# Performance work log

Measured on AMD Instinct MI355X. Metric: run time of the kernel, lower is better.

The kernel has to match this reference:

```python
import jax, jax.numpy as jnp
import numpy as np
from jax import lax

TH = 1.0  # fire threshold (init kwarg th)


def setup_inputs() -> dict:
    key = jax.random.key(0)
    k0, k1, k2 = jax.random.split(key, 3)
    B, T, C = 32, 3000, 512
    hs_pad = jax.random.normal(k0, (B, T, C), dtype=jnp.float32)
    hs_mask = jnp.ones((B, 1, T), dtype=jnp.int32)  # espnet-style [B,1,T] mask, 1=valid
    # Conv1d(C, C, k=5) weight layout [out, in, k], fan-in scaled
    conv_w = jax.random.normal(k1, (C, C, 5), dtype=jnp.float32) * (1.0 / np.sqrt(C * 5))
    conv_b = jnp.zeros((C,), dtype=jnp.float32)
    # Linear(C, 1): stored transposed as [C, 1]
    lin_w = jax.random.normal(k2, (C, 1), dtype=jnp.float32) * (1.0 / np.sqrt(C))
    lin_b = jnp.zeros((1,), dtype=jnp.float32)
    return dict(hs_pad=hs_pad, hs_mask=hs_mask, conv_w=conv_w, conv_b=conv_b,
                lin_w=lin_w, lin_b=lin_b)


def _cif_single(alpha, h, th):
    """Integrate-and-fire for one sequence. alpha:[T], h:[T,C] -> [T,C] (zero padded)."""
    T, C = h.shape

    def step(carry, inp):
        acc, hacc = carry
        a, hu = inp
        acc2 = acc + a
        fired = acc2 >= th
        a1 = th - acc  # = th - (acc2 - a)
        emit = jnp.where(fired, hacc + a1 * hu, jnp.zeros_like(hu))
        new_acc = jnp.where(fired, a - a1, acc2)
        new_h = jnp.where(fired, (a - a1) * hu, hacc + a * hu)
        return (new_acc, new_h), (fired, emit)

    (acc_f, h_f), (fired, emits) = lax.scan(
        step, (jnp.float32(0.0), jnp.zeros((C,), h.dtype)), (alpha, h))
    nfire = jnp.cumsum(fired.astype(jnp.int32))
    idx = jnp.where(fired, nfire - 1, T)  # non-fired steps dump into scratch row T
    out = jnp.zeros((T + 1, C), h.dtype).at[idx].add(emits)
    # tail emission: remaining mass >= th/2
    tail = acc_f >= th * 0.5
    tail_idx = jnp.where(tail, nfire[-1], T)
    out = out.at[tail_idx].add(jnp.where(tail, h_f, jnp.zeros_like(h_f)))
    return out[:T]  # fires <= T always (alpha < 1 = th)


def _forward(hs_pad, hs_mask, conv_w, conv_b, lin_w, lin_b):
    B, T, C = hs_pad.shape
    # Conv1d(C,C,5,pad=2) on [B,C,T]  (note: self.norm is never used in the torch forward)
    x = lax.conv_general_dilated(hs_pad.transpose(0, 2, 1), conv_w, (1,), [(2, 2)],
                                 dimension_numbers=('NCH', 'OIH', 'NCH'))
    x = jax.nn.relu(x + conv_b[None, :, None])  # [B,C,T]
    alpha = jax.nn.sigmoid(jnp.einsum('bct,co->bto', x, lin_w) + lin_b)  # [B,T,1]
    # ys_pad=None -> T_y = 0; loss computed BEFORE masking (as in torch)
    loss_pen = jnp.abs(alpha.sum(axis=1) - 0.0).sum()
    a = alpha[..., 0] * (hs_mask[:, 0, :] != 0).astype(alpha.dtype)  # masked_fill(mask==0, 0)
    cs = jax.vmap(lambda av, hv: _cif_single(av, hv, TH))(a, hs_pad)  # [B,T,C]
    cs_mask = jnp.any(cs != 0.0, axis=-1)[:, None, :]  # [B,1,T]
    return cs, cs_mask, loss_pen


def reference(hs_pad, hs_mask, conv_w, conv_b, lin_w, lin_b):
    return _forward(hs_pad, hs_mask, conv_w, conv_b, lin_w, lin_b)
```

## Files before the change

kernel.cpp:

```cpp
#include <hip/hip_runtime.h>
#include <math.h>

#define B_ 32
#define T_ 3000
#define C_ 512
#define THf 1.0f
#define KW 2560

typedef _Float16 f16;
typedef _Float16 half8 __attribute__((ext_vector_type(8)));
typedef float floatx4 __attribute__((ext_vector_type(4)));

#define GLOBAL_AS __attribute__((address_space(1)))
#define LDS_AS __attribute__((address_space(3)))

#define CS_SIZE  ((size_t)B_ * T_ * C_)
#define MASK_OFF CS_SIZE
#define LOSS_OFF (CS_SIZE + (size_t)B_ * T_)

#define HS16_ELEMS   ((size_t)B_ * 16 * 3000 * 64)
#define HS16_ZEL     HS16_ELEMS
#define HS16_BYTES   (2 * (HS16_ELEMS + 64))
#define A_WHI_OFF    HS16_BYTES
#define A_WLO_OFF    (A_WHI_OFF + 2621440)
#define A_PL_OFF     (A_WLO_OFF + 2621440)
#define A_ALPHA_OFF  (A_PL_OFF + 3072000)
#define A_SEGI_OFF   (A_ALPHA_OFF + 384000)
#define A_SEGW_OFF   (A_SEGI_OFF + 768000)
#define A_TOT_OFF    (A_SEGW_OFF + 768000)
#define A_WS_NEED    (A_TOT_OFF + 128)

#define B_WHI_OFF   0
#define B_WLO_OFF   2621440
#define B_PL_OFF    5242880
#define B_ALPHA_OFF 8314880
#define B_SEGI_OFF  8698880
#define B_SEGW_OFF  9466880
#define B_TOT_OFF   10234880

__global__ __launch_bounds__(256) void w_prep_kernel(
    const float* __restrict__ W, f16* __restrict__ whi, f16* __restrict__ wlo)
{
    int idx = blockIdx.x * 256 + threadIdx.x;
    if (idx >= 512 * KW) return;
    int ie = idx & 7;
    int o  = (idx >> 3) & 511;
    int i8 = (idx >> 12) & 63;
    int k  = idx >> 18;
    int i  = i8 * 8 + ie;
    float w = W[o * KW + i * 5 + k];
    f16 h = (f16)w;
    whi[idx] = h;
    wlo[idx] = (f16)((w - (float)h) * 2048.0f);
}

__global__ __launch_bounds__(256) void hs_split_kernel(
    const float* __restrict__ hs, f16* __restrict__ hs16)
{
    int idx = blockIdx.x * 256 + threadIdx.x;
    if (idx < 8) {
        half8 z = {(f16)0.f, (f16)0.f, (f16)0.f, (f16)0.f,
                   (f16)0.f, (f16)0.f, (f16)0.f, (f16)0.f};
        *(half8*)(hs16 + HS16_ZEL + idx * 8) = z;
    }
    if (idx >= B_ * 16 * 3000 * 4) return;
    int ch  = idx & 3;
    int row = idx >> 2;
    int t   = row % 3000;
    int bic = row / 3000;
    int b   = bic >> 4;
    int ic  = bic & 15;
    const float* src = hs + ((size_t)b * 3000 + t) * 512 + ic * 32 + ch * 8;
    float4 v0 = *(const float4*)src;
    float4 v1 = *(const float4*)(src + 4);
    float vv[8] = {v0.x, v0.y, v0.z, v0.w, v1.x, v1.y, v1.z, v1.w};
    half8 hh, ll;
#pragma unroll
    for (int q = 0; q < 8; ++q) {
        f16 x = (f16)vv[q];
        hh[q] = x;
        ll[q] = (f16)((vv[q] - (float)x) * 2048.f);
    }
    int m7 = (t + 2) & 7;
    size_t rb = (size_t)row * 64;
    *(half8*)(hs16 + rb + (size_t)((ch ^ m7) * 8))       = hh;
    *(half8*)(hs16 + rb + (size_t)(((ch + 4) ^ m7) * 8)) = ll;
}

__global__ __launch_bounds__(256, 2) void conv_alpha_mfma_a(
    const f16* __restrict__ hs16, const f16* __restrict__ whi_g,
    const f16* __restrict__ wlo_g, const float* __restrict__ conv_b,
    const float* __restrict__ lin_w, float* __restrict__ pl)
{
    __shared__ f16 sm[33792];

    int tid = threadIdx.x;
    int bid = blockIdx.x;
    int nb  = bid & 3;
    int mtg = bid >> 2;
    int b   = mtg / 24;
    int mt  = mtg - b * 24;
    int t0  = mt * 128;

    int wid = tid >> 6, l = tid & 63;
    int wm = wid >> 1, wn = wid & 1;
    int l15 = l & 15, l4 = l >> 4;
    int o0 = nb * 128;

    floatx4 acc1[4][4], acc2[4][4];
#pragma unroll
    for (int mf = 0; mf < 4; ++mf)
#pragma unroll
        for (int nf = 0; nf < 4; ++nf) {
            acc1[mf][nf] = (floatx4)0.f;
            acc2[mf][nf] = (floatx4)0.f;
        }

    auto issue_a = [&](int icn) {
        const f16* hbase = hs16 + ((size_t)(b * 16 + icn)) * 3000 * 64;
        f16* abase = sm + (icn & 1) * 8704;
#pragma unroll
        for (int jj = 0; jj < 4; ++jj) {
            int j = wid + jj * 4;
            int r = j * 8 + (l >> 3);
            int t = t0 - 2 + r;
            const f16* gsrc = ((unsigned)t < 3000u)
                ? hbase + (size_t)t * 64 + (l & 7) * 8
                : hs16 + HS16_ZEL + (l & 7) * 8;
            __builtin_amdgcn_global_load_lds((const GLOBAL_AS void*)gsrc,
                                             (LDS_AS void*)(abase + j * 512), 16, 0, 0);
        }
        {
            int j = (wid == 0) ? 16 : (wid + 12);
            int r = j * 8 + (l >> 3);
            int t = t0 - 2 + r;
            const f16* gsrc = ((unsigned)t < 3000u)
                ? hbase + (size_t)t * 64 + (l & 7) * 8
                : hs16 + HS16_ZEL + (l & 7) * 8;
            __builtin_amdgcn_global_load_lds((const GLOBAL_AS void*)gsrc,
                                             (LDS_AS void*)(abase + j * 512), 16, 0, 0);
        }
    };
    auto issue_w = [&](int s2) {
        int buf = s2 & 1;
        int ic2 = s2 / 5, k2 = s2 - ic2 * 5;
#pragma unroll
        for (int rr = 0; rr < 4; ++rr) {
            int r = wid * 4 + rr;
            int arr = r >> 3, kc = (r >> 1) & 3, oh = r & 1;
            const f16* gsrc = (arr ? wlo_g : whi_g) +
                ((size_t)((k2 * 64 + ic2 * 4 + kc) * 512 + o0 + oh * 64 + l)) * 8;
            f16* ldst = sm + 17408 + (buf * 2 + arr) * 4096 + (kc * 128 + oh * 64) * 8;
            __builtin_amdgcn_global_load_lds((const GLOBAL_AS void*)gsrc,
                                             (LDS_AS void*)ldst, 16, 0, 0);
        }
    };

    issue_a(0);
    issue_w(0);
    __syncthreads();

    for (int s = 0; s < 80; ++s) {
        int ic = s / 5, k = s - ic * 5;
        int abuf = ic & 1, wbuf = s & 1;
        bool aStep = (k == 0) && (ic + 1 < 16);

        if (s + 1 < 80) issue_w(s + 1);
        if (aStep) issue_a(ic + 1);

        const f16* Ab = sm + abuf * 8704;
        const f16* Wh = sm + 17408 + (wbuf * 2 + 0) * 4096;
        const f16* Wl = sm + 17408 + (wbuf * 2 + 1) * 4096;
        int m7 = (l15 + k) & 7;
        int sh = (l4 ^ m7) * 8;
        int sl = ((l4 + 4) ^ m7) * 8;

        half8 ah[4], al[4], bh[4], bl[4];
#pragma unroll
        for (int f = 0; f < 4; ++f) {
            int r = wm * 64 + f * 16 + l15 + k;
            ah[f] = *(const half8*)(Ab + r * 64 + sh);
            al[f] = *(const half8*)(Ab + r * 64 + sl);
            int wrow = l4 * 128 + wn * 64 + f * 16 + l15;
            bh[f] = *(const half8*)(Wh + wrow * 8);
            bl[f] = *(const half8*)(Wl + wrow * 8);
        }
        __builtin_amdgcn_s_setprio(1);
#pragma unroll
        for (int mf = 0; mf < 4; ++mf)
#pragma unroll
            for (int nf = 0; nf < 4; ++nf) {
                acc1[mf][nf] = __builtin_amdgcn_mfma_f32_16x16x32_f16(
                    ah[mf], bh[nf], acc1[mf][nf], 0, 0, 0);
                acc2[mf][nf] = __builtin_amdgcn_mfma_f32_16x16x32_f16(
                    al[mf], bh[nf], acc2[mf][nf], 0, 0, 0);
                acc2[mf][nf] = __builtin_amdgcn_mfma_f32_16x16x32_f16(
                    ah[mf], bl[nf], acc2[mf][nf], 0, 0, 0);
            }
        __builtin_amdgcn_s_setprio(0);

        if (aStep) {
            asm volatile("s_waitcnt vmcnt(5)" ::: "memory");
            __builtin_amdgcn_s_barrier();
            __builtin_amdgcn_sched_barrier(0);
        } else {
            __syncthreads();
        }
    }

    float cb[4], lw[4];
#pragma unroll
    for (int nf = 0; nf < 4; ++nf) {
        int o = o0 + wn * 64 + nf * 16 + l15;
        cb[nf] = conv_b[o];
        lw[nf] = lin_w[o];
    }
    float* plb = pl + (size_t)(nb * 2 + wn) * (B_ * T_) + b * T_;
#pragma unroll
    for (int mf = 0; mf < 4; ++mf) {
#pragma unroll
        for (int reg = 0; reg < 4; ++reg) {
            float v = 0.f;
#pragma unroll
            for (int nf = 0; nf < 4; ++nf) {
                float c = acc1[mf][nf][reg] + acc2[mf][nf][reg] * (1.0f / 2048.0f);
                v += fmaxf(c + cb[nf], 0.f) * lw[nf];
            }
            v += __shfl_xor(v, 1);
            v += __shfl_xor(v, 2);
            v += __shfl_xor(v, 4);
            v += __shfl_xor(v, 8);
            int trow = t0 + wm * 64 + mf * 16 + l4 * 4 + reg;
            if (l15 == reg && trow < T_) plb[trow] = v;
        }
    }
}

#define A_ROWS 132
#define ALO_OFF_E  8448
#define WB_OFF_E   16896
#define WB_ARR_E   4096

__global__ __launch_bounds__(256, 2) void conv_alpha_mfma_b(
    const float* __restrict__ hs, const f16* __restrict__ whi_g,
    const f16* __restrict__ wlo_g, const float* __restrict__ conv_b,
    const float* __restrict__ lin_w, float* __restrict__ pl)
{
    __shared__ f16 sm[33280];
    f16* Ahi = sm;
    f16* Alo = sm + ALO_OFF_E;
    f16* Wb  = sm + WB_OFF_E;

    int tid = threadIdx.x;
    int bid = blockIdx.x;
    int nb  = bid & 3;
    int mtg = bid >> 2;
    int b   = mtg / 24;
    int mt  = mtg - b * 24;
    int t0  = mt * 128;

    int wid = tid >> 6, l = tid & 63;
    int wm = wid >> 1, wn = wid & 1;
    int l15 = l & 15, l4 = l >> 4;

    const float* hb = hs + (size_t)b * T_ * C_;
    int o0 = nb * 128;

    floatx4 acc1[4][4], acc2[4][4];
#pragma unroll
    for (int mf = 0; mf < 4; ++mf)
#pragma unroll
        for (int nf = 0; nf < 4; ++nf) {
            acc1[mf][nf] = (floatx4)0.f;
            acc2[mf][nf] = (floatx4)0.f;
        }

    auto issue_w = [&](int s2) {
        int buf = s2 & 1;
        int ic2 = s2 / 10, kk2 = s2 % 10;
        int k2 = kk2 >> 1, sub2 = kk2 & 1;
        int i8b = ic2 * 8 + sub2 * 4;
#pragma unroll
        for (int rr = 0; rr < 4; ++rr) {
            int r = wid * 4 + rr;
            int arr = r >> 3, kc = (r >> 1) & 3, oh = r & 1;
            const f16* gsrc = (arr ? wlo_g : whi_g) +
                ((size_t)((k2 * 64 + i8b + kc) * 512 + o0 + oh * 64 + l)) * 8;
            f16* ldst = Wb + (buf * 2 + arr) * WB_ARR_E + (kc * 128 + oh * 64) * 8;
            __builtin_amdgcn_global_load_lds((const GLOBAL_AS void*)gsrc,
                                             (LDS_AS void*)ldst, 16, 0, 0);
        }
    };

    issue_w(0);

    for (int s = 0; s < 80; ++s) {
        int ic = s / 10, kk = s % 10;
        int k = kk >> 1, sub = kk & 1;
        int buf = s & 1;

        if (kk == 0) {
            int i0 = ic * 64;
            for (int j = tid; j < A_ROWS * 8; j += 256) {
                int r = j >> 3, c = j & 7;
                int t = t0 - 2 + r;
                float4 v0 = make_float4(0.f, 0.f, 0.f, 0.f);
                float4 v1 = v0;
                if ((unsigned)t < (unsigned)T_) {
                    const float4* p = (const float4*)(hb + (size_t)t * C_ + i0 + c * 8);
                    v0 = p[0]; v1 = p[1];
                }
                float vv[8] = {v0.x, v0.y, v0.z, v0.w, v1.x, v1.y, v1.z, v1.w};
                half8 hh, ll;
#pragma unroll
                for (int q = 0; q < 8; ++q) {
                    f16 x = (f16)vv[q];
                    hh[q] = x;
                    ll[q] = (f16)((vv[q] - (float)x) * 2048.f);
                }
                int off = r * 64 + (c ^ (r & 7)) * 8;
                *(half8*)(Ahi + off) = hh;
                *(half8*)(Alo + off) = ll;
            }
            __syncthreads();
        }

        if (s + 1 < 80) issue_w(s + 1);

        half8 ah[4], al[4], bh[4], bl[4];
#pragma unroll
        for (int f = 0; f < 4; ++f) {
            int ar = wm * 64 + f * 16 + l15 + k;
            int aoff = ar * 64 + ((((sub << 2) | l4) ^ (ar & 7)) << 3);
            ah[f] = *(const half8*)(Ahi + aoff);
            al[f] = *(const half8*)(Alo + aoff);
            int wrow = l4 * 128 + wn * 64 + f * 16 + l15;
            bh[f] = *(const half8*)(Wb + (buf * 2 + 0) * WB_ARR_E + wrow * 8);
            bl[f] = *(const half8*)(Wb + (buf * 2 + 1) * WB_ARR_E + wrow * 8);
        }
        __builtin_amdgcn_s_setprio(1);
#pragma unroll
        for (int mf = 0; mf < 4; ++mf)
#pragma unroll
            for (int nf = 0; nf < 4; ++nf) {
                acc1[mf][nf] = __builtin_amdgcn_mfma_f32_16x16x32_f16(
                    ah[mf], bh[nf], acc1[mf][nf], 0, 0, 0);
                acc2[mf][nf] = __builtin_amdgcn_mfma_f32_16x16x32_f16(
                    al[mf], bh[nf], acc2[mf][nf], 0, 0, 0);
                acc2[mf][nf] = __builtin_amdgcn_mfma_f32_16x16x32_f16(
                    ah[mf], bl[nf], acc2[mf][nf], 0, 0, 0);
            }
        __builtin_amdgcn_s_setprio(0);
        __syncthreads();
    }

    float cb[4], lw[4];
#pragma unroll
    for (int nf = 0; nf < 4; ++nf) {
        int o = o0 + wn * 64 + nf * 16 + l15;
        cb[nf] = conv_b[o];
        lw[nf] = lin_w[o];
    }
    float* plb = pl + (size_t)(nb * 2 + wn) * (B_ * T_) + b * T_;
#pragma unroll
    for (int mf = 0; mf < 4; ++mf) {
#pragma unroll
        for (int reg = 0; reg < 4; ++reg) {
            float v = 0.f;
#pragma unroll
            for (int nf = 0; nf < 4; ++nf) {
                float c = acc1[mf][nf][reg] + acc2[mf][nf][reg] * (1.0f / 2048.0f);
                v += fmaxf(c + cb[nf], 0.f) * lw[nf];
            }
            v += __shfl_xor(v, 1);
            v += __shfl_xor(v, 2);
            v += __shfl_xor(v, 4);
            v += __shfl_xor(v, 8);
            int trow = t0 + wm * 64 + mf * 16 + l4 * 4 + reg;
            if (l15 == reg && trow < T_) plb[trow] = v;
        }
    }
}

__global__ __launch_bounds__(256) void alpha_combine_kernel(
    const float* __restrict__ pl, const float* __restrict__ lin_b,
    float* __restrict__ alpha)
{
    int idx = blockIdx.x * 256 + threadIdx.x;
    if (idx >= B_ * T_) return;
    float s = lin_b[0];
#pragma unroll
    for (int p = 0; p < 8; ++p) s += pl[(size_t)p * (B_ * T_) + idx];
    alpha[idx] = 1.f / (1.f + expf(-s));
}

__global__ __launch_bounds__(64) void scan_kernel(
    float* __restrict__ alpha, const int* __restrict__ mask,
    int2* __restrict__ seg_i, float2* __restrict__ seg_w,
    int* __restrict__ total_rows, float* __restrict__ out_loss)
{
    int lane = threadIdx.x;
    float lsum = 0.f;
    if (lane < B_) {
        const float4* ap = (const float4*)(alpha + lane * T_);
        const int4*   mp = (const int4*)(mask + lane * T_);
        float* astore = alpha + lane * T_;
        int2*   si = seg_i + lane * T_;
        float2* sw = seg_w + lane * T_;

        float acc = 0.f, leftover = 0.f;
        int nf = 0, prev_t = -1;

        float4 c0 = ap[0], c1 = ap[1];
        int4   m0 = mp[0], m1 = mp[1];
        for (int tc = 0; tc < T_ / 8; ++tc) {
            float4 n0, n1; int4 nm0, nm1;
            if (tc + 1 < T_ / 8) {
                n0 = ap[(tc + 1) * 2]; n1 = ap[(tc + 1) * 2 + 1];
                nm0 = mp[(tc + 1) * 2]; nm1 = mp[(tc + 1) * 2 + 1];
            }
            float av[8] = {c0.x, c0.y, c0.z, c0.w, c1.x, c1.y, c1.z, c1.w};
            int   mv[8] = {m0.x, m0.y, m0.z, m0.w, m1.x, m1.y, m1.z, m1.w};
#pragma unroll
            for (int u = 0; u < 8; ++u) {
                int t = tc * 8 + u;
                float araw = av[u];
                lsum += araw;
                float a = (mv[u] != 0) ? araw : 0.f;
                astore[t] = a;
                float acc2 = acc + a;
                float a1 = THf - acc;
                if (acc2 >= THf) {
                    si[nf] = make_int2(prev_t, t);
                    sw[nf] = make_float2(leftover, a1);
                    float rem = a - a1;
                    leftover = rem;
                    acc = rem;
                    prev_t = t;
                    ++nf;
                } else {
                    acc = acc2;
                }
            }
            c0 = n0; c1 = n1; m0 = nm0; m1 = nm1;
        }
        int tot = nf;
        if (acc >= 0.5f * THf) {
            si[nf] = make_int2(prev_t, T_);
            sw[nf] = make_float2(leftover, 0.f);
            ++tot;
        }
        total_rows[lane] = tot;
        lsum = fabsf(lsum);
    }
#pragma unroll
    for (int off = 16; off >= 1; off >>= 1) lsum += __shfl_down(lsum, off);
    if (lane == 0) out_loss[0] = lsum;
}

__global__ __launch_bounds__(128) void emit_kernel(
    const float* __restrict__ hs, const float* __restrict__ alpha,
    const int2* __restrict__ seg_i, const float2* __restrict__ seg_w,
    const int* __restrict__ total_rows, float* __restrict__ out)
{
    int blk = blockIdx.x;
    int b = blk / T_;
    int r = blk % T_;
    int tid = threadIdx.x;

    float4* cs4 = (float4*)(out + ((size_t)b * T_ + r) * C_);
    float* maskp = out + MASK_OFF + (size_t)b * T_ + r;
    int tot = total_rows[b];

    if (r >= tot) {
        float4 z; z.x = 0.f; z.y = 0.f; z.z = 0.f; z.w = 0.f;
        cs4[tid] = z;
        if (tid == 0) *maskp = 0.f;
        return;
    }
    int2   si = seg_i[b * T_ + r];
    float2 sw = seg_w[b * T_ + r];
    const float4* hb = (const float4*)(hs + (size_t)b * T_ * C_);
    const float*  ab = alpha + b * T_;

    float4 acc; acc.x = 0.f; acc.y = 0.f; acc.z = 0.f; acc.w = 0.f;
    int ts = si.x, te = si.y;
    if (ts >= 0) {
        float4 h = hb[(size_t)ts * (C_ / 4) + tid];
        acc.x = sw.x * h.x; acc.y = sw.x * h.y; acc.z = sw.x * h.z; acc.w = sw.x * h.w;
    }
    for (int t = ts + 1; t < te; ++t) {
        float a = ab[t];
        float4 h = hb[(size_t)t * (C_ / 4) + tid];
        acc.x = fmaf(a, h.x, acc.x); acc.y = fmaf(a, h.y, acc.y);
        acc.z = fmaf(a, h.z, acc.z); acc.w = fmaf(a, h.w, acc.w);
    }
    if (te < T_) {
        float4 h = hb[(size_t)te * (C_ / 4) + tid];
        acc.x = fmaf(sw.y, h.x, acc.x); acc.y = fmaf(sw.y, h.y, acc.y);
        acc.z = fmaf(sw.y, h.z, acc.z); acc.w = fmaf(sw.y, h.w, acc.w);
    }
    cs4[tid] = acc;
    if (tid == 0) *maskp = 1.f;
}

extern "C" void kernel_launch(void* const* d_in, const int* in_sizes, int n_in,
                              void* d_out, int out_size, void* d_ws, size_t ws_size,
                              hipStream_t stream)
{
    const float* hs     = (const float*)d_in[0];
    const int*   hmask  = (const int*)d_in[1];
    const float* conv_w = (const float*)d_in[2];
    const float* conv_b = (const float*)d_in[3];
    const float* lin_w  = (const float*)d_in[4];
    const float* lin_b  = (const float*)d_in[5];
    float* out = (float*)d_out;
    char*  ws  = (char*)d_ws;

    if (ws_size >= (size_t)A_WS_NEED) {
        f16*    hs16  = (f16*)ws;
        f16*    whi   = (f16*)(ws + A_WHI_OFF);
        f16*    wlo   = (f16*)(ws + A_WLO_OFF);
        float*  pl    = (float*)(ws + A_PL_OFF);
        float*  alpha = (float*)(ws + A_ALPHA_OFF);
        int2*   seg_i = (int2*)(ws + A_SEGI_OFF);
        float2* seg_w = (float2*)(ws + A_SEGW_OFF);
        int*    tot   = (int*)(ws + A_TOT_OFF);

        w_prep_kernel<<<(512 * KW + 255) / 256, 256, 0, stream>>>(conv_w, whi, wlo);
        hs_split_kernel<<<(B_ * 16 * 3000 * 4 + 255) / 256, 256, 0, stream>>>(hs, hs16);
        conv_alpha_mfma_a<<<B_ * 24 * 4, 256, 0, stream>>>(hs16, whi, wlo, conv_b,
                                                           lin_w, pl);
        alpha_combine_kernel<<<(B_ * T_ + 255) / 256, 256, 0, stream>>>(pl, lin_b, alpha);
        scan_kernel<<<1, 64, 0, stream>>>(alpha, hmask, seg_i, seg_w, tot, out + LOSS_OFF);
        emit_kernel<<<B_ * T_, 128, 0, stream>>>(hs, alpha, seg_i, seg_w, tot, out);
    } else {
        f16*    whi   = (f16*)(ws + B_WHI_OFF);
        f16*    wlo   = (f16*)(ws + B_WLO_OFF);
        float*  pl    = (float*)(ws + B_PL_OFF);
        float*  alpha = (float*)(ws + B_ALPHA_OFF);
        int2*   seg_i = (int2*)(ws + B_SEGI_OFF);
        float2* seg_w = (float2*)(ws + B_SEGW_OFF);
        int*    tot   = (int*)(ws + B_TOT_OFF);

        w_prep_kernel<<<(512 * KW + 255) / 256, 256, 0, stream>>>(conv_w, whi, wlo);
        conv_alpha_mfma_b<<<B_ * 24 * 4, 256, 0, stream>>>(hs, whi, wlo, conv_b,
                                                           lin_w, pl);
        alpha_combine_kernel<<<(B_ * T_ + 255) / 256, 256, 0, stream>>>(pl, lin_b, alpha);
        scan_kernel<<<1, 64, 0, stream>>>(alpha, hmask, seg_i, seg_w, tot, out + LOSS_OFF);
        emit_kernel<<<B_ * T_, 128, 0, stream>>>(hs, alpha, seg_i, seg_w, tot, out);
    }
}
```

Baseline: 994.4 us.

## Switch conv MFMA to 32x32x16 tiles with single accumulator and occupancy 3

```diff
diff --git a/kernel.cpp b/kernel.cpp
--- a/kernel.cpp
+++ b/kernel.cpp
@@ -10,6 +10,7 @@
 typedef _Float16 f16;
 typedef _Float16 half8 __attribute__((ext_vector_type(8)));
 typedef float floatx4 __attribute__((ext_vector_type(4)));
+typedef float floatx16 __attribute__((ext_vector_type(16)));
 
 #define GLOBAL_AS __attribute__((address_space(1)))
 #define LDS_AS __attribute__((address_space(3)))
@@ -17,6 +18,8 @@
 #define CS_SIZE  ((size_t)B_ * T_ * C_)
 #define MASK_OFF CS_SIZE
 #define LOSS_OFF (CS_SIZE + (size_t)B_ * T_)
+
+#define LOSC 64.0f
 
 #define HS16_ELEMS   ((size_t)B_ * 16 * 3000 * 64)
 #define HS16_ZEL     HS16_ELEMS
@@ -51,7 +54,7 @@
     float w = W[o * KW + i * 5 + k];
     f16 h = (f16)w;
     whi[idx] = h;
-    wlo[idx] = (f16)((w - (float)h) * 2048.0f);
+    wlo[idx] = (f16)((w - (float)h) * LOSC);
 }
 
 __global__ __launch_bounds__(256) void hs_split_kernel(
@@ -79,7 +82,7 @@
     for (int q = 0; q < 8; ++q) {
         f16 x = (f16)vv[q];
         hh[q] = x;
-        ll[q] = (f16)((vv[q] - (float)x) * 2048.f);
+        ll[q] = (f16)((vv[q] - (float)x) * LOSC);
     }
     int m7 = (t + 2) & 7;
     size_t rb = (size_t)row * 64;
@@ -87,12 +90,12 @@
     *(half8*)(hs16 + rb + (size_t)(((ch + 4) ^ m7) * 8)) = ll;
 }
 
-__global__ __launch_bounds__(256, 2) void conv_alpha_mfma_a(
+__global__ __launch_bounds__(256, 3) void conv_alpha_mfma_a(
     const f16* __restrict__ hs16, const f16* __restrict__ whi_g,
     const f16* __restrict__ wlo_g, const float* __restrict__ conv_b,
     const float* __restrict__ lin_w, float* __restrict__ pl)
 {
-    __shared__ f16 sm[33792];
+    __shared__ f16 sm[25600];
 
     int tid = threadIdx.x;
     int bid = blockIdx.x;
@@ -104,17 +107,14 @@
 
     int wid = tid >> 6, l = tid & 63;
     int wm = wid >> 1, wn = wid & 1;
-    int l15 = l & 15, l4 = l >> 4;
+    int l31 = l & 31, l5 = l >> 5;
     int o0 = nb * 128;
 
-    floatx4 acc1[4][4], acc2[4][4];
-#pragma unroll
-    for (int mf = 0; mf < 4; ++mf)
-#pragma unroll
-        for (int nf = 0; nf < 4; ++nf) {
-            acc1[mf][nf] = (floatx4)0.f;
-            acc2[mf][nf] = (floatx4)0.f;
-        }
+    floatx16 acc[2][2];
+#pragma unroll
+    for (int mf = 0; mf < 2; ++mf)
+#pragma unroll
+        for (int nf = 0; nf < 2; ++nf) acc[mf][nf] = (floatx16)0.f;
 
     auto issue_a = [&](int icn) {
         const f16* hbase = hs16 + ((size_t)(b * 16 + icn)) * 3000 * 64;
@@ -142,15 +142,16 @@
         }
     };
     auto issue_w = [&](int s2) {
-        int buf = s2 & 1;
-        int ic2 = s2 / 5, k2 = s2 - ic2 * 5;
-#pragma unroll
-        for (int rr = 0; rr < 4; ++rr) {
-            int r = wid * 4 + rr;
-            int arr = r >> 3, kc = (r >> 1) & 3, oh = r & 1;
-            const f16* gsrc = (arr ? wlo_g : whi_g) +
-                ((size_t)((k2 * 64 + ic2 * 4 + kc) * 512 + o0 + oh * 64 + l)) * 8;
-            f16* ldst = sm + 17408 + (buf * 2 + arr) * 4096 + (kc * 128 + oh * 64) * 8;
+        int wbuf2 = s2 & 1;
+        int ic2 = s2 / 10, kk2 = s2 % 10;
+        int k2 = kk2 >> 1, h2 = kk2 & 1;
+        int g0 = ic2 * 4 + h2 * 2;
+        int g = wid >> 1, oh = wid & 1;
+#pragma unroll
+        for (int v = 0; v < 2; ++v) {
+            const f16* gsrc = (v ? wlo_g : whi_g) +
+                ((size_t)((k2 * 64 + g0 + g) * 512 + o0 + oh * 64 + l)) * 8;
+            f16* ldst = sm + 17408 + wbuf2 * 4096 + ((v * 2 + g) * 128 + oh * 64) * 8;
             __builtin_amdgcn_global_load_lds((const GLOBAL_AS void*)gsrc,
                                              (LDS_AS void*)ldst, 16, 0, 0);
         }
@@ -160,78 +161,72 @@
     issue_w(0);
     __syncthreads();
 
-    for (int s = 0; s < 80; ++s) {
-        int ic = s / 5, k = s - ic * 5;
+    const f16 inv64 = (f16)(1.0f / 64.0f);
+
+    for (int s = 0; s < 160; ++s) {
+        int ic = s / 10, kk = s % 10;
+        int k = kk >> 1, h = kk & 1;
         int abuf = ic & 1, wbuf = s & 1;
-        bool aStep = (k == 0) && (ic + 1 < 16);
-
-        if (s + 1 < 80) issue_w(s + 1);
-        if (aStep) issue_a(ic + 1);
+
+        if (s + 1 < 160) issue_w(s + 1);
+        if (kk == 0 && ic + 1 < 16) issue_a(ic + 1);
 
         const f16* Ab = sm + abuf * 8704;
-        const f16* Wh = sm + 17408 + (wbuf * 2 + 0) * 4096;
-        const f16* Wl = sm + 17408 + (wbuf * 2 + 1) * 4096;
-        int m7 = (l15 + k) & 7;
-        int sh = (l4 ^ m7) * 8;
-        int sl = ((l4 + 4) ^ m7) * 8;
-
-        half8 ah[4], al[4], bh[4], bl[4];
-#pragma unroll
-        for (int f = 0; f < 4; ++f) {
-            int r = wm * 64 + f * 16 + l15 + k;
-            ah[f] = *(const half8*)(Ab + r * 64 + sh);
-            al[f] = *(const half8*)(Ab + r * 64 + sl);
-            int wrow = l4 * 128 + wn * 64 + f * 16 + l15;
-            bh[f] = *(const half8*)(Wh + wrow * 8);
-            bl[f] = *(const half8*)(Wl + wrow * 8);
-        }
+        const f16* Wb = sm + 17408 + wbuf * 4096;
+        int chh = h * 2 + l5;
+
+        half8 ah[2], al[2], bh[2], bl[2];
+#pragma unroll
+        for (int f = 0; f < 2; ++f) {
+            int r = wm * 64 + f * 32 + l31 + k;
+            int sw = r & 7;
+            ah[f] = *(const half8*)(Ab + r * 64 + ((chh ^ sw) << 3));
+            al[f] = *(const half8*)(Ab + r * 64 + (((chh + 4) ^ sw) << 3));
+            int oin = wn * 64 + f * 32 + l31;
+            bh[f] = *(const half8*)(Wb + (l5 * 128 + oin) * 8);
+            bl[f] = *(const half8*)(Wb + ((2 + l5) * 128 + oin) * 8);
+        }
+        half8 ahd[2], bhd[2];
+#pragma unroll
+        for (int f = 0; f < 2; ++f) { ahd[f] = ah[f] * inv64; bhd[f] = bh[f] * inv64; }
+
         __builtin_amdgcn_s_setprio(1);
 #pragma unroll
-        for (int mf = 0; mf < 4; ++mf)
-#pragma unroll
-            for (int nf = 0; nf < 4; ++nf) {
-                acc1[mf][nf] = __builtin_amdgcn_mfma_f32_16x16x32_f16(
-                    ah[mf], bh[nf], acc1[mf][nf], 0, 0, 0);
-                acc2[mf][nf] = __builtin_amdgcn_mfma_f32_16x16x32_f16(
-                    al[mf], bh[nf], acc2[mf][nf], 0, 0, 0);
-                acc2[mf][nf] = __builtin_amdgcn_mfma_f32_16x16x32_f16(
-                    ah[mf], bl[nf], acc2[mf][nf], 0, 0, 0);
+        for (int mf = 0; mf < 2; ++mf)
+#pragma unroll
+            for (int nf = 0; nf < 2; ++nf) {
+                acc[mf][nf] = __builtin_amdgcn_mfma_f32_32x32x16_f16(
+                    ah[mf], bh[nf], acc[mf][nf], 0, 0, 0);
+                acc[mf][nf] = __builtin_amdgcn_mfma_f32_32x32x16_f16(
+                    al[mf], bhd[nf], acc[mf][nf], 0, 0, 0);
+                acc[mf][nf] = __builtin_amdgcn_mfma_f32_32x32x16_f16(
+                    ahd[mf], bl[nf], acc[mf][nf], 0, 0, 0);
             }
         __builtin_amdgcn_s_setprio(0);
-
-        if (aStep) {
-            asm volatile("s_waitcnt vmcnt(5)" ::: "memory");
-            __builtin_amdgcn_s_barrier();
-            __builtin_amdgcn_sched_barrier(0);
-        } else {
-            __syncthreads();
-        }
-    }
-
-    float cb[4], lw[4];
-#pragma unroll
-    for (int nf = 0; nf < 4; ++nf) {
-        int o = o0 + wn * 64 + nf * 16 + l15;
+        __syncthreads();
+    }
+
+    float cb[2], lw[2];
+#pragma unroll
+    for (int nf = 0; nf < 2; ++nf) {
+        int o = o0 + wn * 64 + nf * 32 + l31;
         cb[nf] = conv_b[o];
         lw[nf] = lin_w[o];
     }
     float* plb = pl + (size_t)(nb * 2 + wn) * (B_ * T_) + b * T_;
 #pragma unroll
-    for (int mf = 0; mf < 4; ++mf) {
-#pragma unroll
-        for (int reg = 0; reg < 4; ++reg) {
-            float v = 0.f;
-#pragma unroll
-            for (int nf = 0; nf < 4; ++nf) {
-                float c = acc1[mf][nf][reg] + acc2[mf][nf][reg] * (1.0f / 2048.0f);
-                v += fmaxf(c + cb[nf], 0.f) * lw[nf];
-            }
+    for (int mf = 0; mf < 2; ++mf) {
+#pragma unroll
+        for (int r = 0; r < 16; ++r) {
+            float v = fmaxf(acc[mf][0][r] + cb[0], 0.f) * lw[0]
+                    + fmaxf(acc[mf][1][r] + cb[1], 0.f) * lw[1];
             v += __shfl_xor(v, 1);
             v += __shfl_xor(v, 2);
             v += __shfl_xor(v, 4);
             v += __shfl_xor(v, 8);
-            int trow = t0 + wm * 64 + mf * 16 + l4 * 4 + reg;
-            if (l15 == reg && trow < T_) plb[trow] = v;
+            v += __shfl_xor(v, 16);
+            int trow = t0 + wm * 64 + mf * 32 + l5 * 4 + (r & 3) + 8 * (r >> 2);
+            if (l31 == 0 && trow < T_) plb[trow] = v;
         }
     }
 }
@@ -316,7 +311,7 @@
                 for (int q = 0; q < 8; ++q) {
                     f16 x = (f16)vv[q];
                     hh[q] = x;
-                    ll[q] = (f16)((vv[q] - (float)x) * 2048.f);
+                    ll[q] = (f16)((vv[q] - (float)x) * LOSC);
                 }
                 int off = r * 64 + (c ^ (r & 7)) * 8;
                 *(half8*)(Ahi + off) = hh;
@@ -369,7 +364,7 @@
             float v = 0.f;
 #pragma unroll
             for (int nf = 0; nf < 4; ++nf) {
-                float c = acc1[mf][nf][reg] + acc2[mf][nf][reg] * (1.0f / 2048.0f);
+                float c = acc1[mf][nf][reg] + acc2[mf][nf][reg] * (1.0f / LOSC);
                 v += fmaxf(c + cb[nf], 0.f) * lw[nf];
             }
             v += __shfl_xor(v, 1);
```

Measured after the change: 1.153 ms. 1.16x slower.

## Merge split-fp16 accumulators and single-buffer A tile to raise conv kernel occupancy

Applied to the files above, without the earlier changes.

```diff
diff --git a/kernel.cpp b/kernel.cpp
--- a/kernel.cpp
+++ b/kernel.cpp
@@ -17,6 +17,8 @@
 #define CS_SIZE  ((size_t)B_ * T_ * C_)
 #define MASK_OFF CS_SIZE
 #define LOSS_OFF (CS_SIZE + (size_t)B_ * T_)
+
+#define LOSC 64.0f
 
 #define HS16_ELEMS   ((size_t)B_ * 16 * 3000 * 64)
 #define HS16_ZEL     HS16_ELEMS
@@ -51,7 +53,7 @@
     float w = W[o * KW + i * 5 + k];
     f16 h = (f16)w;
     whi[idx] = h;
-    wlo[idx] = (f16)((w - (float)h) * 2048.0f);
+    wlo[idx] = (f16)((w - (float)h) * LOSC);
 }
 
 __global__ __launch_bounds__(256) void hs_split_kernel(
@@ -79,7 +81,7 @@
     for (int q = 0; q < 8; ++q) {
         f16 x = (f16)vv[q];
         hh[q] = x;
-        ll[q] = (f16)((vv[q] - (float)x) * 2048.f);
+        ll[q] = (f16)((vv[q] - (float)x) * LOSC);
     }
     int m7 = (t + 2) & 7;
     size_t rb = (size_t)row * 64;
@@ -87,12 +89,12 @@
     *(half8*)(hs16 + rb + (size_t)(((ch + 4) ^ m7) * 8)) = ll;
 }
 
-__global__ __launch_bounds__(256, 2) void conv_alpha_mfma_a(
+__global__ __launch_bounds__(256, 3) void conv_alpha_mfma_a(
     const f16* __restrict__ hs16, const f16* __restrict__ whi_g,
     const f16* __restrict__ wlo_g, const float* __restrict__ conv_b,
     const float* __restrict__ lin_w, float* __restrict__ pl)
 {
-    __shared__ f16 sm[33792];
+    __shared__ f16 sm[25088];
 
     int tid = threadIdx.x;
     int bid = blockIdx.x;
@@ -107,18 +109,15 @@
     int l15 = l & 15, l4 = l >> 4;
     int o0 = nb * 128;
 
-    floatx4 acc1[4][4], acc2[4][4];
+    floatx4 acc[4][4];
 #pragma unroll
     for (int mf = 0; mf < 4; ++mf)
 #pragma unroll
-        for (int nf = 0; nf < 4; ++nf) {
-            acc1[mf][nf] = (floatx4)0.f;
-            acc2[mf][nf] = (floatx4)0.f;
-        }
+        for (int nf = 0; nf < 4; ++nf) acc[mf][nf] = (floatx4)0.f;
 
     auto issue_a = [&](int icn) {
         const f16* hbase = hs16 + ((size_t)(b * 16 + icn)) * 3000 * 64;
-        f16* abase = sm + (icn & 1) * 8704;
+        f16* abase = sm;
 #pragma unroll
         for (int jj = 0; jj < 4; ++jj) {
             int j = wid + jj * 4;
@@ -150,7 +149,7 @@
             int arr = r >> 3, kc = (r >> 1) & 3, oh = r & 1;
             const f16* gsrc = (arr ? wlo_g : whi_g) +
                 ((size_t)((k2 * 64 + ic2 * 4 + kc) * 512 + o0 + oh * 64 + l)) * 8;
-            f16* ldst = sm + 17408 + (buf * 2 + arr) * 4096 + (kc * 128 + oh * 64) * 8;
+            f16* ldst = sm + 8704 + (buf * 2 + arr) * 4096 + (kc * 128 + oh * 64) * 8;
             __builtin_amdgcn_global_load_lds((const GLOBAL_AS void*)gsrc,
                                              (LDS_AS void*)ldst, 16, 0, 0);
         }
@@ -160,17 +159,18 @@
     issue_w(0);
     __syncthreads();
 
+    const f16 inv64 = (f16)0.015625f;
+
     for (int s = 0; s < 80; ++s) {
         int ic = s / 5, k = s - ic * 5;
-        int abuf = ic & 1, wbuf = s & 1;
-        bool aStep = (k == 0) && (ic + 1 < 16);
-
-        if (s + 1 < 80) issue_w(s + 1);
-        if (aStep) issue_a(ic + 1);
-
-        const f16* Ab = sm + abuf * 8704;
-        const f16* Wh = sm + 17408 + (wbuf * 2 + 0) * 4096;
-        const f16* Wl = sm + 17408 + (wbuf * 2 + 1) * 4096;
+        int wbuf = s & 1;
+        bool aStep = (k == 4);
+
+        if (!aStep && s + 1 < 80) issue_w(s + 1);
+
+        const f16* Ab = sm;
+        const f16* Wh = sm + 8704 + (wbuf * 2 + 0) * 4096;
+        const f16* Wl = sm + 8704 + (wbuf * 2 + 1) * 4096;
         int m7 = (l15 + k) & 7;
         int sh = (l4 ^ m7) * 8;
         int sl = ((l4 + 4) ^ m7) * 8;
@@ -185,24 +185,31 @@
             bh[f] = *(const half8*)(Wh + wrow * 8);
             bl[f] = *(const half8*)(Wl + wrow * 8);
         }
+        half8 bhd[4];
+#pragma unroll
+        for (int nf = 0; nf < 4; ++nf) bhd[nf] = bh[nf] * inv64;
+
         __builtin_amdgcn_s_setprio(1);
 #pragma unroll
-        for (int mf = 0; mf < 4; ++mf)
+        for (int mf = 0; mf < 4; ++mf) {
+            half8 ahd = ah[mf] * inv64;
 #pragma unroll
             for (int nf = 0; nf < 4; ++nf) {
-                acc1[mf][nf] = __builtin_amdgcn_mfma_f32_16x16x32_f16(
-                    ah[mf], bh[nf], acc1[mf][nf], 0, 0, 0);
-                acc2[mf][nf] = __builtin_amdgcn_mfma_f32_16x16x32_f16(
-                    al[mf], bh[nf], acc2[mf][nf], 0, 0, 0);
-                acc2[mf][nf] = __builtin_amdgcn_mfma_f32_16x16x32_f16(
-                    ah[mf], bl[nf], acc2[mf][nf], 0, 0, 0);
-            }
+                acc[mf][nf] = __builtin_amdgcn_mfma_f32_16x16x32_f16(
+                    ah[mf], bh[nf], acc[mf][nf], 0, 0, 0);
+                acc[mf][nf] = __builtin_amdgcn_mfma_f32_16x16x32_f16(
+                    al[mf], bhd[nf], acc[mf][nf], 0, 0, 0);
+                acc[mf][nf] = __builtin_amdgcn_mfma_f32_16x16x32_f16(
+                    ahd, bl[nf], acc[mf][nf], 0, 0, 0);
+            }
+        }
         __builtin_amdgcn_s_setprio(0);
 
         if (aStep) {
-            asm volatile("s_waitcnt vmcnt(5)" ::: "memory");
-            __builtin_amdgcn_s_barrier();
-            __builtin_amdgcn_sched_barrier(0);
+            __syncthreads();
+            if (ic + 1 < 16) issue_a(ic + 1);
+            if (s + 1 < 80) issue_w(s + 1);
+            __syncthreads();
         } else {
             __syncthreads();
         }
@@ -223,7 +230,7 @@
             float v = 0.f;
 #pragma unroll
             for (int nf = 0; nf < 4; ++nf) {
-                float c = acc1[mf][nf][reg] + acc2[mf][nf][reg] * (1.0f / 2048.0f);
+                float c = acc[mf][nf][reg];
                 v += fmaxf(c + cb[nf], 0.f) * lw[nf];
             }
             v += __shfl_xor(v, 1);
@@ -316,7 +323,7 @@
                 for (int q = 0; q < 8; ++q) {
                     f16 x = (f16)vv[q];
                     hh[q] = x;
-                    ll[q] = (f16)((vv[q] - (float)x) * 2048.f);
+                    ll[q] = (f16)((vv[q] - (float)x) * LOSC);
                 }
                 int off = r * 64 + (c ^ (r & 7)) * 8;
                 *(half8*)(Ahi + off) = hh;
@@ -369,7 +376,7 @@
             float v = 0.f;
 #pragma unroll
             for (int nf = 0; nf < 4; ++nf) {
-                float c = acc1[mf][nf][reg] + acc2[mf][nf][reg] * (1.0f / 2048.0f);
+                float c = acc1[mf][nf][reg] + acc2[mf][nf][reg] * (1.0f / LOSC);
                 v += fmaxf(c + cb[nf], 0.f) * lw[nf];
             }
             v += __shfl_xor(v, 1);
```

Measured after the change: 1.173 ms. 1.18x slower.
